# Kernel optimization log

Hardware: AMD Instinct MI355X
Metric: run time of the kernel (lower is better)

Reference implementation:

```python
import jax, jax.numpy as jnp
import numpy as np

D_MODEL = 768
MIMO_RANK = 4


def setup_inputs() -> dict:
    key = jax.random.key(0)
    ks = jax.random.split(key, 6)
    B, T, D, R = 2, 2048, D_MODEL, MIMO_RANK
    x = jax.random.normal(ks[0], (B, T, D), dtype=jnp.float32)
    norm_w = jnp.ones((D,), dtype=jnp.float32)
    W_in = jax.random.normal(ks[1], (D * R * 2, D), dtype=jnp.float32) * 0.02
    W_out = jax.random.normal(ks[2], (D, D), dtype=jnp.float32) * 0.02
    a_param = jax.random.normal(ks[3], (D, R, 2), dtype=jnp.float32) * 0.12
    b_param = jax.random.normal(ks[4], (D, R, 2), dtype=jnp.float32) * 0.15
    c_param = jax.random.normal(ks[5], (D, R, 2), dtype=jnp.float32) * 0.15
    return {"x": x, "norm_w": norm_w, "W_in": W_in, "W_out": W_out,
            "a_param": a_param, "b_param": b_param, "c_param": c_param}


def reference(x, norm_w, W_in, W_out, a_param, b_param, c_param):
    B, T, D = x.shape
    R = a_param.shape[1]
    # RMSNorm
    xn = x * jax.lax.rsqrt(jnp.mean(x * x, axis=-1, keepdims=True) + 1e-6) * norm_w
    # in_proj -> interleaved complex MIMO input u: [B,T,D,R,2]
    u = (xn @ W_in.T).reshape(B, T, D, R, 2)
    # coefficients (tanh-bounded; |a| scaled by 0.97 for stability)
    a = jnp.tanh(a_param) * 0.97
    b = jnp.tanh(b_param)
    c = jnp.tanh(c_param)
    ac = jax.lax.complex(a[..., 0], a[..., 1])  # [D,R]
    bc = jax.lax.complex(b[..., 0], b[..., 1])
    cc = jax.lax.complex(c[..., 0], c[..., 1])
    uc = jax.lax.complex(u[..., 0], u[..., 1])  # [B,T,D,R]
    # linear complex recurrence s_t = a * s_{t-1} + b * u_t, zero init state,
    # parallelized with an associative scan over time.
    bu = bc[None, None] * uc
    A = jnp.broadcast_to(ac[None, None], bu.shape)

    def comb(l, r):
        return (l[0] * r[0], r[0] * l[1] + r[1])

    _, s = jax.lax.associative_scan(comb, (A, bu), axis=1)  # [B,T,D,R] complex
    # output mix: real part of c * h, summed over MIMO rank -> [B,T,D]
    y = jnp.real(cc[None, None] * s).sum(axis=-1)
    return y @ W_out.T
```

## Files before the change

### kernel.cpp

```cpp
#include <hip/hip_runtime.h>
#include <hip/hip_bf16.h>
#include <stdint.h>

#define BATCH 2
#define TT 2048
#define DM 768
#define RR 4
#define M_TOK 4096
#define NFEAT 6144
#define NCH 6144
#define CHUNK 64
#define NCHUNK 32

typedef __attribute__((ext_vector_type(8))) short short8;
typedef __attribute__((ext_vector_type(4))) float float4v;

__device__ inline float bf2f(uint32_t bits16) {
    union { uint32_t u; float f; } x; x.u = bits16 << 16; return x.f;
}

typedef const __attribute__((address_space(1))) void* gptr_t;
typedef __attribute__((address_space(3))) void* lptr_t;

__device__ inline void async_ld16(const void* g, void* l) {
    __builtin_amdgcn_global_load_lds((gptr_t)(uintptr_t)g, (lptr_t)(uintptr_t)l,
                                     16, 0, 0);
}

__device__ inline void store_c(__hip_bfloat16* C, size_t idx, float v) {
    C[idx] = __float2bfloat16(v);
}
__device__ inline void store_c(float* C, size_t idx, float v) { C[idx] = v; }

__device__ inline uint2 pack4bf(float a, float b, float c, float d) {
    union { __hip_bfloat16 h[4]; uint2 u; } o;
    o.h[0] = __float2bfloat16(a); o.h[1] = __float2bfloat16(b);
    o.h[2] = __float2bfloat16(c); o.h[3] = __float2bfloat16(d);
    return o.u;
}

__global__ __launch_bounds__(256) void prep_kernel(
    const float* __restrict__ W_in, const float* __restrict__ W_out,
    const float* __restrict__ ap, const float* __restrict__ bp,
    const float* __restrict__ cp,
    __hip_bfloat16* __restrict__ Win_bf, __hip_bfloat16* __restrict__ Wout_bf,
    float2* __restrict__ ac, float2* __restrict__ bc,
    float2* __restrict__ cc, float2* __restrict__ aL) {
    const int N1 = NFEAT * DM / 4;
    const int N2 = DM * DM / 4;
    int i = blockIdx.x * 256 + threadIdx.x;
    if (i < N1) {
        float4 v = ((const float4*)W_in)[i];
        ((uint2*)Win_bf)[i] = pack4bf(v.x, v.y, v.z, v.w);
    } else if (i < N1 + N2) {
        int k = i - N1;
        float4 v = ((const float4*)W_out)[k];
        ((uint2*)Wout_bf)[k] = pack4bf(v.x, v.y, v.z, v.w);
    }
    if (i < DM * RR) {
        float ar = tanhf(ap[2 * i])     * 0.97f;
        float ai = tanhf(ap[2 * i + 1]) * 0.97f;
        ac[i] = make_float2(ar, ai);
        bc[i] = make_float2(tanhf(bp[2 * i]), tanhf(bp[2 * i + 1]));
        cc[i] = make_float2(tanhf(cp[2 * i]), tanhf(cp[2 * i + 1]));
        float xr = ar, xi = ai;
        #pragma unroll
        for (int k = 0; k < 6; ++k) {
            float nr = xr * xr - xi * xi;
            float ni = 2.f * xr * xi;
            xr = nr; xi = ni;
        }
        aL[i] = make_float2(xr, xi);
    }
}

__global__ __launch_bounds__(192) void rmsnorm_kernel(
    const float* __restrict__ x, const float* __restrict__ w,
    __hip_bfloat16* __restrict__ xn) {
    int row = blockIdx.x;
    int tid = threadIdx.x;
    float4 v = ((const float4*)(x + (size_t)row * DM))[tid];
    float ss = v.x * v.x + v.y * v.y + v.z * v.z + v.w * v.w;
    #pragma unroll
    for (int o = 1; o < 64; o <<= 1) ss += __shfl_xor(ss, o);
    __shared__ float wsum[3];
    if ((tid & 63) == 0) wsum[tid >> 6] = ss;
    __syncthreads();
    float tot = wsum[0] + wsum[1] + wsum[2];
    float scale = rsqrtf(tot * (1.f / DM) + 1e-6f);
    float4 wv = ((const float4*)w)[tid];
    ((uint2*)(xn + (size_t)row * DM))[tid] =
        pack4bf(v.x * scale * wv.x, v.y * scale * wv.y,
                v.z * scale * wv.z, v.w * scale * wv.w);
}

template <int BM, int BN, int BK, typename OutT>
__device__ inline void gemm_body(
    const __hip_bfloat16* __restrict__ A, const __hip_bfloat16* __restrict__ B,
    OutT* __restrict__ C, int M, int N, int K) {
    constexpr int MI = BM / 32;
    constexpr int NJ = BN / 32;
    constexpr int CPR = BK / 8;
    __shared__ __attribute__((aligned(16))) __hip_bfloat16 lA[BM * BK];
    __shared__ __attribute__((aligned(16))) __hip_bfloat16 lB[BN * BK];
    const int tid  = threadIdx.x;
    const int lane = tid & 63;
    const int wave = tid >> 6;
    const int quad = lane >> 4;
    const int l15  = lane & 15;
    const int wm = (wave >> 1) * (BM / 2);
    const int wn = (wave & 1) * (BN / 2);
    const int m0 = blockIdx.y * BM;
    const int n0 = blockIdx.x * BN;

    float4v acc[MI][NJ] = {};

    for (int k0 = 0; k0 < K; k0 += BK) {
        __syncthreads();
        #pragma unroll
        for (int it = 0; it < BM * CPR / 256; ++it) {
            int p = it * 256 + tid;
            int row = p / CPR;
            int cg = (p & (CPR - 1)) ^ (row & (CPR - 1));
            async_ld16(A + (size_t)(m0 + row) * K + k0 + cg * 8, lA + p * 8);
        }
        #pragma unroll
        for (int it = 0; it < BN * CPR / 256; ++it) {
            int p = it * 256 + tid;
            int row = p / CPR;
            int cg = (p & (CPR - 1)) ^ (row & (CPR - 1));
            async_ld16(B + (size_t)(n0 + row) * K + k0 + cg * 8, lB + p * 8);
        }
        __syncthreads();
        #pragma unroll
        for (int s = 0; s < BK / 32; ++s) {
            short8 af[MI], bfr[NJ];
            #pragma unroll
            for (int i = 0; i < MI; ++i) {
                int r = wm + i * 16 + l15;
                int c = (s * 4 + quad) ^ (r & (CPR - 1));
                af[i] = *(const short8*)(lA + r * BK + c * 8);
            }
            #pragma unroll
            for (int j = 0; j < NJ; ++j) {
                int r = wn + j * 16 + l15;
                int c = (s * 4 + quad) ^ (r & (CPR - 1));
                bfr[j] = *(const short8*)(lB + r * BK + c * 8);
            }
            #pragma unroll
            for (int i = 0; i < MI; ++i)
                #pragma unroll
                for (int j = 0; j < NJ; ++j)
                    acc[i][j] = __builtin_amdgcn_mfma_f32_16x16x32_bf16(
                        af[i], bfr[j], acc[i][j], 0, 0, 0);
        }
    }
    #pragma unroll
    for (int i = 0; i < MI; ++i)
        #pragma unroll
        for (int j = 0; j < NJ; ++j)
            #pragma unroll
            for (int rg = 0; rg < 4; ++rg) {
                int row = m0 + wm + i * 16 + quad * 4 + rg;
                int col = n0 + wn + j * 16 + l15;
                store_c(C, (size_t)row * N + col, acc[i][j][rg]);
            }
}

__global__ __launch_bounds__(256) void gemm_in(
    const __hip_bfloat16* __restrict__ A, const __hip_bfloat16* __restrict__ B,
    __hip_bfloat16* __restrict__ C, int M, int N, int K) {
    gemm_body<128, 128, 64, __hip_bfloat16>(A, B, C, M, N, K);
}

__global__ __launch_bounds__(256) void gemm_out(
    const __hip_bfloat16* __restrict__ A, const __hip_bfloat16* __restrict__ B,
    float* __restrict__ C, int M, int N, int K) {
    gemm_body<64, 64, 128, float>(A, B, C, M, N, K);
}

__device__ inline void cstep(float& sr, float& si, float2 a, float2 bb,
                             uint32_t uw) {
    float ur = bf2f(uw & 0xffffu), ui = bf2f(uw >> 16);
    float tr = bb.x * ur - bb.y * ui;
    float ti = bb.x * ui + bb.y * ur;
    float nr = a.x * sr - a.y * si + tr;
    float ni = a.x * si + a.y * sr + ti;
    sr = nr; si = ni;
}

__global__ __launch_bounds__(256) void scan_passA(
    const uint4* __restrict__ u4,
    const float2* __restrict__ ac, const float2* __restrict__ bc,
    float2* __restrict__ chunkEnd) {
    int g = blockIdx.x * 256 + threadIdx.x;
    int j = blockIdx.y;
    int b = g >= DM;
    int d = g - b * DM;
    int cb = d * RR;
    float2 a0 = ac[cb], a1 = ac[cb + 1], a2 = ac[cb + 2], a3 = ac[cb + 3];
    float2 b0 = bc[cb], b1 = bc[cb + 1], b2 = bc[cb + 2], b3 = bc[cb + 3];
    float s0r = 0, s0i = 0, s1r = 0, s1i = 0;
    float s2r = 0, s2i = 0, s3r = 0, s3i = 0;
    size_t base = ((size_t)(b * TT + j * CHUNK)) * DM + d;
    #pragma unroll 4
    for (int i = 0; i < CHUNK; ++i) {
        uint4 uw = u4[base + (size_t)i * DM];
        cstep(s0r, s0i, a0, b0, uw.x);
        cstep(s1r, s1i, a1, b1, uw.y);
        cstep(s2r, s2i, a2, b2, uw.z);
        cstep(s3r, s3i, a3, b3, uw.w);
    }
    size_t eb = (size_t)j * NCH + b * (DM * RR) + cb;
    chunkEnd[eb]     = make_float2(s0r, s0i);
    chunkEnd[eb + 1] = make_float2(s1r, s1i);
    chunkEnd[eb + 2] = make_float2(s2r, s2i);
    chunkEnd[eb + 3] = make_float2(s3r, s3i);
}

__global__ __launch_bounds__(256) void scan_passB(
    const float2* __restrict__ chunkEnd, const float2* __restrict__ aLp,
    float2* __restrict__ carry) {
    int c = blockIdx.x * 256 + threadIdx.x;
    int rem = (c >= DM * RR) ? c - DM * RR : c;
    float2 aL = aLp[rem];
    float sr = 0.f, si = 0.f;
    for (int j = 0; j < NCHUNK; ++j) {
        carry[(size_t)j * NCH + c] = make_float2(sr, si);
        float2 e = chunkEnd[(size_t)j * NCH + c];
        float nr = aL.x * sr - aL.y * si + e.x;
        float ni = aL.x * si + aL.y * sr + e.y;
        sr = nr; si = ni;
    }
}

__global__ __launch_bounds__(256) void scan_passC(
    const uint4* __restrict__ u4,
    const float2* __restrict__ ac, const float2* __restrict__ bc,
    const float2* __restrict__ cc, const float2* __restrict__ carry,
    __hip_bfloat16* __restrict__ y) {
    int g = blockIdx.x * 256 + threadIdx.x;
    int j = blockIdx.y;
    int b = g >= DM;
    int d = g - b * DM;
    int cb = d * RR;
    float2 a0 = ac[cb], a1 = ac[cb + 1], a2 = ac[cb + 2], a3 = ac[cb + 3];
    float2 b0 = bc[cb], b1 = bc[cb + 1], b2 = bc[cb + 2], b3 = bc[cb + 3];
    float2 c0 = cc[cb], c1 = cc[cb + 1], c2 = cc[cb + 2], c3 = cc[cb + 3];
    size_t kb = (size_t)j * NCH + b * (DM * RR) + cb;
    float2 k0 = carry[kb], k1 = carry[kb + 1];
    float2 k2 = carry[kb + 2], k3 = carry[kb + 3];
    float s0r = k0.x, s0i = k0.y, s1r = k1.x, s1i = k1.y;
    float s2r = k2.x, s2i = k2.y, s3r = k3.x, s3i = k3.y;
    size_t base  = ((size_t)(b * TT + j * CHUNK)) * DM + d;
    #pragma unroll 4
    for (int i = 0; i < CHUNK; ++i) {
        uint4 uw = u4[base + (size_t)i * DM];
        cstep(s0r, s0i, a0, b0, uw.x);
        cstep(s1r, s1i, a1, b1, uw.y);
        cstep(s2r, s2i, a2, b2, uw.z);
        cstep(s3r, s3i, a3, b3, uw.w);
        float yv = c0.x * s0r - c0.y * s0i + c1.x * s1r - c1.y * s1i
                 + c2.x * s2r - c2.y * s2i + c3.x * s3r - c3.y * s3i;
        y[base + (size_t)i * DM] = __float2bfloat16(yv);
    }
}

extern "C" void kernel_launch(void* const* d_in, const int* in_sizes, int n_in,
                              void* d_out, int out_size, void* d_ws,
                              size_t ws_size, hipStream_t stream) {
    const float* x      = (const float*)d_in[0];
    const float* norm_w = (const float*)d_in[1];
    const float* W_in   = (const float*)d_in[2];
    const float* W_out  = (const float*)d_in[3];
    const float* a_p    = (const float*)d_in[4];
    const float* b_p    = (const float*)d_in[5];
    const float* c_p    = (const float*)d_in[6];
    float* out = (float*)d_out;

    char* ws = (char*)d_ws;
    size_t off = 0;
    auto alloc = [&](size_t bytes) {
        void* p = ws + off;
        off += (bytes + 255) & ~(size_t)255;
        return p;
    };
    __hip_bfloat16* Win_bf  = (__hip_bfloat16*)alloc((size_t)NFEAT * DM * 2);
    __hip_bfloat16* Wout_bf = (__hip_bfloat16*)alloc((size_t)DM * DM * 2);
    __hip_bfloat16* xn      = (__hip_bfloat16*)alloc((size_t)M_TOK * DM * 2);
    __hip_bfloat16* u       = (__hip_bfloat16*)alloc((size_t)M_TOK * NFEAT * 2);
    __hip_bfloat16* y       = (__hip_bfloat16*)alloc((size_t)M_TOK * DM * 2);
    float2* ac = (float2*)alloc((size_t)DM * RR * 8);
    float2* bc = (float2*)alloc((size_t)DM * RR * 8);
    float2* cc = (float2*)alloc((size_t)DM * RR * 8);
    float2* aL = (float2*)alloc((size_t)DM * RR * 8);
    float2* chunkEnd = (float2*)alloc((size_t)NCHUNK * NCH * 8);
    float2* carry    = (float2*)alloc((size_t)NCHUNK * NCH * 8);

    {
        int n_total = (NFEAT * DM + DM * DM) / 4;
        prep_kernel<<<(n_total + 255) / 256, 256, 0, stream>>>(
            W_in, W_out, a_p, b_p, c_p, Win_bf, Wout_bf, ac, bc, cc, aL);
    }
    rmsnorm_kernel<<<M_TOK, 192, 0, stream>>>(x, norm_w, xn);
    gemm_in<<<dim3(NFEAT / 128, M_TOK / 128), 256, 0, stream>>>(
        xn, Win_bf, u, M_TOK, NFEAT, DM);
    scan_passA<<<dim3(BATCH * DM / 256, NCHUNK), 256, 0, stream>>>(
        (const uint4*)u, ac, bc, chunkEnd);
    scan_passB<<<NCH / 256, 256, 0, stream>>>(chunkEnd, aL, carry);
    scan_passC<<<dim3(BATCH * DM / 256, NCHUNK), 256, 0, stream>>>(
        (const uint4*)u, ac, bc, cc, carry, y);
    gemm_out<<<dim3(DM / 64, M_TOK / 64), 256, 0, stream>>>(
        y, Wout_bf, out, M_TOK, DM, DM);
}
```

Baseline: 192.7 us.

## Fuse rmsnorm into prep, fold carry scan into passC, split in-proj GEMM

Merges the RMSNorm into the weight-cast prep kernel as extra blocks, removing one launch. It drops the separate carry-propagation kernel: each passC block now recomputes its incoming carry by serially combining the preceding chunk-end states. The input GEMM is split into two launches over halves of the output features, which halves the grid of each launch. This removes launches and the carry buffer, at the cost of redundant serial carry work in passC (up to 31 steps per thread) and an extra GEMM launch.

```diff
diff --git a/kernel.cpp b/kernel.cpp
--- a/kernel.cpp
+++ b/kernel.cpp
@@ -39,16 +39,39 @@
     return o.u;
 }
 
-__global__ __launch_bounds__(256) void prep_kernel(
+__global__ __launch_bounds__(256) void prep_rms(
+    const float* __restrict__ x, const float* __restrict__ w,
     const float* __restrict__ W_in, const float* __restrict__ W_out,
     const float* __restrict__ ap, const float* __restrict__ bp,
     const float* __restrict__ cp,
+    __hip_bfloat16* __restrict__ xn,
     __hip_bfloat16* __restrict__ Win_bf, __hip_bfloat16* __restrict__ Wout_bf,
     float2* __restrict__ ac, float2* __restrict__ bc,
     float2* __restrict__ cc, float2* __restrict__ aL) {
+    int bid = blockIdx.x;
+    int tid = threadIdx.x;
+    if (bid < M_TOK) {
+        __shared__ float wsum[3];
+        float4 v = make_float4(0.f, 0.f, 0.f, 0.f);
+        if (tid < 192) v = ((const float4*)(x + (size_t)bid * DM))[tid];
+        float ss = v.x * v.x + v.y * v.y + v.z * v.z + v.w * v.w;
+        #pragma unroll
+        for (int o = 1; o < 64; o <<= 1) ss += __shfl_xor(ss, o);
+        if (tid < 192 && (tid & 63) == 0) wsum[tid >> 6] = ss;
+        __syncthreads();
+        if (tid < 192) {
+            float tot = wsum[0] + wsum[1] + wsum[2];
+            float scale = rsqrtf(tot * (1.f / DM) + 1e-6f);
+            float4 wv = ((const float4*)w)[tid];
+            ((uint2*)(xn + (size_t)bid * DM))[tid] =
+                pack4bf(v.x * scale * wv.x, v.y * scale * wv.y,
+                        v.z * scale * wv.z, v.w * scale * wv.w);
+        }
+        return;
+    }
     const int N1 = NFEAT * DM / 4;
     const int N2 = DM * DM / 4;
-    int i = blockIdx.x * 256 + threadIdx.x;
+    int i = (bid - M_TOK) * 256 + tid;
     if (i < N1) {
         float4 v = ((const float4*)W_in)[i];
         ((uint2*)Win_bf)[i] = pack4bf(v.x, v.y, v.z, v.w);
@@ -74,30 +97,10 @@
     }
 }
 
-__global__ __launch_bounds__(192) void rmsnorm_kernel(
-    const float* __restrict__ x, const float* __restrict__ w,
-    __hip_bfloat16* __restrict__ xn) {
-    int row = blockIdx.x;
-    int tid = threadIdx.x;
-    float4 v = ((const float4*)(x + (size_t)row * DM))[tid];
-    float ss = v.x * v.x + v.y * v.y + v.z * v.z + v.w * v.w;
-    #pragma unroll
-    for (int o = 1; o < 64; o <<= 1) ss += __shfl_xor(ss, o);
-    __shared__ float wsum[3];
-    if ((tid & 63) == 0) wsum[tid >> 6] = ss;
-    __syncthreads();
-    float tot = wsum[0] + wsum[1] + wsum[2];
-    float scale = rsqrtf(tot * (1.f / DM) + 1e-6f);
-    float4 wv = ((const float4*)w)[tid];
-    ((uint2*)(xn + (size_t)row * DM))[tid] =
-        pack4bf(v.x * scale * wv.x, v.y * scale * wv.y,
-                v.z * scale * wv.z, v.w * scale * wv.w);
-}
-
 template <int BM, int BN, int BK, typename OutT>
 __device__ inline void gemm_body(
     const __hip_bfloat16* __restrict__ A, const __hip_bfloat16* __restrict__ B,
-    OutT* __restrict__ C, int M, int N, int K) {
+    OutT* __restrict__ C, int K, int ldc, int n0base) {
     constexpr int MI = BM / 32;
     constexpr int NJ = BN / 32;
     constexpr int CPR = BK / 8;
@@ -111,7 +114,7 @@
     const int wm = (wave >> 1) * (BM / 2);
     const int wn = (wave & 1) * (BN / 2);
     const int m0 = blockIdx.y * BM;
-    const int n0 = blockIdx.x * BN;
+    const int n0 = n0base + blockIdx.x * BN;
 
     float4v acc[MI][NJ] = {};
 
@@ -163,20 +166,25 @@
             for (int rg = 0; rg < 4; ++rg) {
                 int row = m0 + wm + i * 16 + quad * 4 + rg;
                 int col = n0 + wn + j * 16 + l15;
-                store_c(C, (size_t)row * N + col, acc[i][j][rg]);
+                store_c(C, (size_t)row * ldc + col, acc[i][j][rg]);
             }
 }
 
-__global__ __launch_bounds__(256) void gemm_in(
+__global__ __launch_bounds__(256) void gemm_in_a(
     const __hip_bfloat16* __restrict__ A, const __hip_bfloat16* __restrict__ B,
-    __hip_bfloat16* __restrict__ C, int M, int N, int K) {
-    gemm_body<128, 128, 64, __hip_bfloat16>(A, B, C, M, N, K);
+    __hip_bfloat16* __restrict__ C, int K) {
+    gemm_body<128, 128, 64, __hip_bfloat16>(A, B, C, K, NFEAT, 0);
+}
+__global__ __launch_bounds__(256) void gemm_in_b(
+    const __hip_bfloat16* __restrict__ A, const __hip_bfloat16* __restrict__ B,
+    __hip_bfloat16* __restrict__ C, int K) {
+    gemm_body<128, 128, 64, __hip_bfloat16>(A, B, C, K, NFEAT, NFEAT / 2);
 }
 
 __global__ __launch_bounds__(256) void gemm_out(
     const __hip_bfloat16* __restrict__ A, const __hip_bfloat16* __restrict__ B,
-    float* __restrict__ C, int M, int N, int K) {
-    gemm_body<64, 64, 128, float>(A, B, C, M, N, K);
+    float* __restrict__ C, int K) {
+    gemm_body<64, 64, 128, float>(A, B, C, K, DM, 0);
 }
 
 __device__ inline void cstep(float& sr, float& si, float2 a, float2 bb,
@@ -218,26 +226,11 @@
     chunkEnd[eb + 3] = make_float2(s3r, s3i);
 }
 
-__global__ __launch_bounds__(256) void scan_passB(
-    const float2* __restrict__ chunkEnd, const float2* __restrict__ aLp,
-    float2* __restrict__ carry) {
-    int c = blockIdx.x * 256 + threadIdx.x;
-    int rem = (c >= DM * RR) ? c - DM * RR : c;
-    float2 aL = aLp[rem];
-    float sr = 0.f, si = 0.f;
-    for (int j = 0; j < NCHUNK; ++j) {
-        carry[(size_t)j * NCH + c] = make_float2(sr, si);
-        float2 e = chunkEnd[(size_t)j * NCH + c];
-        float nr = aL.x * sr - aL.y * si + e.x;
-        float ni = aL.x * si + aL.y * sr + e.y;
-        sr = nr; si = ni;
-    }
-}
-
 __global__ __launch_bounds__(256) void scan_passC(
     const uint4* __restrict__ u4,
     const float2* __restrict__ ac, const float2* __restrict__ bc,
-    const float2* __restrict__ cc, const float2* __restrict__ carry,
+    const float2* __restrict__ cc, const float2* __restrict__ aLp,
+    const float2* __restrict__ chunkEnd,
     __hip_bfloat16* __restrict__ y) {
     int g = blockIdx.x * 256 + threadIdx.x;
     int j = blockIdx.y;
@@ -247,12 +240,20 @@
     float2 a0 = ac[cb], a1 = ac[cb + 1], a2 = ac[cb + 2], a3 = ac[cb + 3];
     float2 b0 = bc[cb], b1 = bc[cb + 1], b2 = bc[cb + 2], b3 = bc[cb + 3];
     float2 c0 = cc[cb], c1 = cc[cb + 1], c2 = cc[cb + 2], c3 = cc[cb + 3];
-    size_t kb = (size_t)j * NCH + b * (DM * RR) + cb;
-    float2 k0 = carry[kb], k1 = carry[kb + 1];
-    float2 k2 = carry[kb + 2], k3 = carry[kb + 3];
-    float s0r = k0.x, s0i = k0.y, s1r = k1.x, s1i = k1.y;
-    float s2r = k2.x, s2i = k2.y, s3r = k3.x, s3i = k3.y;
-    size_t base  = ((size_t)(b * TT + j * CHUNK)) * DM + d;
+    float2 aL0 = aLp[cb], aL1 = aLp[cb + 1], aL2 = aLp[cb + 2], aL3 = aLp[cb + 3];
+    float s0r = 0, s0i = 0, s1r = 0, s1i = 0;
+    float s2r = 0, s2i = 0, s3r = 0, s3i = 0;
+    for (int jj = 0; jj < j; ++jj) {
+        size_t eb = (size_t)jj * NCH + b * (DM * RR) + cb;
+        float2 e0 = chunkEnd[eb],     e1 = chunkEnd[eb + 1];
+        float2 e2 = chunkEnd[eb + 2], e3 = chunkEnd[eb + 3];
+        float nr, ni;
+        nr = aL0.x * s0r - aL0.y * s0i + e0.x; ni = aL0.x * s0i + aL0.y * s0r + e0.y; s0r = nr; s0i = ni;
+        nr = aL1.x * s1r - aL1.y * s1i + e1.x; ni = aL1.x * s1i + aL1.y * s1r + e1.y; s1r = nr; s1i = ni;
+        nr = aL2.x * s2r - aL2.y * s2i + e2.x; ni = aL2.x * s2i + aL2.y * s2r + e2.y; s2r = nr; s2i = ni;
+        nr = aL3.x * s3r - aL3.y * s3i + e3.x; ni = aL3.x * s3i + aL3.y * s3r + e3.y; s3r = nr; s3i = ni;
+    }
+    size_t base = ((size_t)(b * TT + j * CHUNK)) * DM + d;
     #pragma unroll 4
     for (int i = 0; i < CHUNK; ++i) {
         uint4 uw = u4[base + (size_t)i * DM];
@@ -295,21 +296,21 @@
     float2* cc = (float2*)alloc((size_t)DM * RR * 8);
     float2* aL = (float2*)alloc((size_t)DM * RR * 8);
     float2* chunkEnd = (float2*)alloc((size_t)NCHUNK * NCH * 8);
-    float2* carry    = (float2*)alloc((size_t)NCHUNK * NCH * 8);
 
     {
-        int n_total = (NFEAT * DM + DM * DM) / 4;
-        prep_kernel<<<(n_total + 255) / 256, 256, 0, stream>>>(
-            W_in, W_out, a_p, b_p, c_p, Win_bf, Wout_bf, ac, bc, cc, aL);
-    }
-    rmsnorm_kernel<<<M_TOK, 192, 0, stream>>>(x, norm_w, xn);
-    gemm_in<<<dim3(NFEAT / 128, M_TOK / 128), 256, 0, stream>>>(
-        xn, Win_bf, u, M_TOK, NFEAT, DM);
+        int cast_blocks = ((NFEAT * DM + DM * DM) / 4 + 255) / 256;
+        prep_rms<<<M_TOK + cast_blocks, 256, 0, stream>>>(
+            x, norm_w, W_in, W_out, a_p, b_p, c_p,
+            xn, Win_bf, Wout_bf, ac, bc, cc, aL);
+    }
+    gemm_in_a<<<dim3(NFEAT / 256, M_TOK / 128), 256, 0, stream>>>(
+        xn, Win_bf, u, DM);
+    gemm_in_b<<<dim3(NFEAT / 256, M_TOK / 128), 256, 0, stream>>>(
+        xn, Win_bf, u, DM);
     scan_passA<<<dim3(BATCH * DM / 256, NCHUNK), 256, 0, stream>>>(
         (const uint4*)u, ac, bc, chunkEnd);
-    scan_passB<<<NCH / 256, 256, 0, stream>>>(chunkEnd, aL, carry);
     scan_passC<<<dim3(BATCH * DM / 256, NCHUNK), 256, 0, stream>>>(
-        (const uint4*)u, ac, bc, cc, carry, y);
+        (const uint4*)u, ac, bc, cc, aL, chunkEnd, y);
     gemm_out<<<dim3(DM / 64, M_TOK / 64), 256, 0, stream>>>(
-        y, Wout_bf, out, M_TOK, DM, DM);
-}
+        y, Wout_bf, out, DM);
+}
```

Result: slower. 202.1 us (+4.9%).
